# Kernel tuning notes

Hardware: AMD Instinct MI355X
Metric: run time of the kernel (lower is better)

## Reference

```python
import jax, jax.numpy as jnp
import numpy as np

NUM_GRAPHS = 1000


def _gine_conv(x, src, dst, edge_attr, w_e, b_e, w1, b1, w2, b2):
    # GINEConv (eps=0): out = nn(x + sum_{j->i} relu(x_j + lin_edge(e_ji)))
    e = edge_attr @ w_e + b_e                      # [E, F]
    m = jax.nn.relu(x[src] + e)                    # [E, F] per-edge message
    agg = jnp.zeros_like(x).at[dst].add(m)         # [N, F] scatter-add to targets
    h = x + agg
    h = jax.nn.relu(h @ w1 + b1)
    h = jax.nn.relu(h @ w2 + b2)
    return h


def _segment_softmax(scores, seg, num_segments):
    m = jax.ops.segment_max(scores, seg, num_segments=num_segments)
    z = jnp.exp(scores - m[seg])
    s = jax.ops.segment_sum(z, seg, num_segments=num_segments)
    return z / s[seg]


def setup_inputs() -> dict:
    key = jax.random.key(0)
    ks = jax.random.split(key, 16)
    N, E, F_IN, H, ED = 100000, 1600000, 9, 64, 1

    x = jax.random.normal(ks[0], (N, F_IN), dtype=jnp.float32)
    edge_index = jax.random.randint(ks[1], (2, E), 0, N, dtype=jnp.int32)
    edge_attr = jax.random.normal(ks[2], (E, ED), dtype=jnp.float32)
    batch = jnp.sort(jax.random.randint(ks[3], (N,), 0, NUM_GRAPHS, dtype=jnp.int32))
    B_total = jax.random.uniform(ks[4], (NUM_GRAPHS,), dtype=jnp.float32)

    def lin(k, fi, fo):
        k1, k2 = jax.random.split(k)
        bound = 1.0 / np.sqrt(fi)
        w = jax.random.uniform(k1, (fi, fo), minval=-bound, maxval=bound, dtype=jnp.float32)
        b = jax.random.uniform(k2, (fo,), minval=-bound, maxval=bound, dtype=jnp.float32)
        return w, b

    we1, be1 = lin(ks[5], ED, F_IN)    # conv1 edge projection -> in_channels
    w11, b11 = lin(ks[6], F_IN, H)
    w12, b12 = lin(ks[7], H, H)
    we2, be2 = lin(ks[8], ED, H)       # conv2 edge projection
    w21, b21 = lin(ks[9], H, H)
    w22, b22 = lin(ks[10], H, H)
    wr1, br1 = lin(ks[11], H, H // 2)
    wr2, br2 = lin(ks[12], H // 2, 1)

    return {"x": x, "edge_index": edge_index, "edge_attr": edge_attr,
            "batch": batch, "B_total": B_total,
            "we1": we1, "be1": be1, "w11": w11, "b11": b11, "w12": w12, "b12": b12,
            "we2": we2, "be2": be2, "w21": w21, "b21": b21, "w22": w22, "b22": b22,
            "wr1": wr1, "br1": br1, "wr2": wr2, "br2": br2}


def reference(x, edge_index, edge_attr, batch, B_total,
              we1, be1, w11, b11, w12, b12,
              we2, be2, w21, b21, w22, b22,
              wr1, br1, wr2, br2):
    src, dst = edge_index[0], edge_index[1]
    h = _gine_conv(x, src, dst, edge_attr, we1, be1, w11, b11, w12, b12)
    h = _gine_conv(h, src, dst, edge_attr, we2, be2, w21, b21, w22, b22)
    raw = (jax.nn.relu(h @ wr1 + br1) @ wr2 + br2)[:, 0]   # [N]
    alloc_probs = _segment_softmax(raw, batch, NUM_GRAPHS)
    return alloc_probs * B_total[batch]
```

## Files before the change

kernel.cpp:

```cpp
#include <hip/hip_runtime.h>
#include <float.h>

#define NBKCAP 128
#define EPB 8192

__device__ __forceinline__ unsigned short bf16rne(float f) {
  unsigned u = __float_as_uint(f);
  return (unsigned short)((u + 0x7FFFu + ((u >> 16) & 1u)) >> 16);
}

__global__ void bkhist_kernel(const int* __restrict__ dst, int* __restrict__ bkcount,
                              int E, int nbk) {
  __shared__ int lcnt[NBKCAP];
  for (int t = threadIdx.x; t < nbk; t += 256) lcnt[t] = 0;
  __syncthreads();
  for (int j = blockIdx.x * 256 + threadIdx.x; j < E; j += gridDim.x * 256)
    atomicAdd(&lcnt[dst[j] >> 10], 1);
  __syncthreads();
  for (int t = threadIdx.x; t < nbk; t += 256)
    if (lcnt[t]) atomicAdd(&bkcount[t], lcnt[t]);
}

__global__ void bkscan_kernel(const int* __restrict__ bkcount, int* __restrict__ bkbase,
                              int* __restrict__ bkcursor, int nbk, int E) {
  if (threadIdx.x == 0) {
    int run = 0;
    for (int i = 0; i < nbk; ++i) { bkbase[i] = run; bkcursor[i] = run; run += bkcount[i]; }
    bkbase[nbk] = E;
  }
}

__global__ void binA_kernel(const int* __restrict__ dst, const int* __restrict__ src,
                            const float* __restrict__ ea,
                            int* __restrict__ bkcursor, int4* __restrict__ epk4,
                            int E, int nbk) {
  __shared__ int lcnt[NBKCAP];
  __shared__ int lbase[NBKCAP];
  int e0 = blockIdx.x * EPB;
  int e1 = min(e0 + EPB, E);
  for (int t = threadIdx.x; t < nbk; t += 256) lcnt[t] = 0;
  __syncthreads();
  for (int j = e0 + threadIdx.x; j < e1; j += 256)
    atomicAdd(&lcnt[dst[j] >> 10], 1);
  __syncthreads();
  for (int t = threadIdx.x; t < nbk; t += 256) {
    int c = lcnt[t];
    lbase[t] = c ? atomicAdd(&bkcursor[t], c) : 0;
    lcnt[t] = 0;
  }
  __syncthreads();
  for (int j = e0 + threadIdx.x; j < e1; j += 256) {
    int d = dst[j];
    int bk = d >> 10;
    int ofs = atomicAdd(&lcnt[bk], 1);
    epk4[lbase[bk] + ofs] = make_int4(src[j], __float_as_int(ea[j]), d, 0);
  }
}

__global__ void bucket_build(const int4* __restrict__ epk4, const int* __restrict__ bkbase,
                             int* __restrict__ rowptr, int2* __restrict__ epack,
                             int N, int E) {
  __shared__ int ldeg[1024];
  __shared__ int lsum[256];
  int bk = blockIdx.x;
  int node0 = bk << 10;
  int s0 = bkbase[bk], s1 = bkbase[bk + 1];
  for (int t = threadIdx.x; t < 1024; t += 256) ldeg[t] = 0;
  __syncthreads();
  for (int p = s0 + threadIdx.x; p < s1; p += 256)
    atomicAdd(&ldeg[epk4[p].z & 1023], 1);
  __syncthreads();
  int base = threadIdx.x * 4;
  int v0 = ldeg[base], v1 = ldeg[base + 1], v2 = ldeg[base + 2], v3 = ldeg[base + 3];
  int s = v0 + v1 + v2 + v3;
  lsum[threadIdx.x] = s;
  __syncthreads();
  for (int off = 1; off < 256; off <<= 1) {
    int t = (threadIdx.x >= off) ? lsum[threadIdx.x - off] : 0;
    __syncthreads();
    lsum[threadIdx.x] += t;
    __syncthreads();
  }
  int ex = lsum[threadIdx.x] - s;
  __syncthreads();
  ldeg[base]     = s0 + ex;
  ldeg[base + 1] = s0 + ex + v0;
  ldeg[base + 2] = s0 + ex + v0 + v1;
  ldeg[base + 3] = s0 + ex + v0 + v1 + v2;
  __syncthreads();
  for (int t = threadIdx.x; t < 1024; t += 256) {
    int node = node0 + t;
    if (node < N) rowptr[node] = ldeg[t];
  }
  __syncthreads();
  for (int p = s0 + threadIdx.x; p < s1; p += 256) {
    int4 v = epk4[p];
    int pos = atomicAdd(&ldeg[v.z & 1023], 1);
    epack[pos] = make_int2(v.x, v.y);
  }
  if (bk == 0 && threadIdx.x == 0) rowptr[N] = E;
}

__global__ void __launch_bounds__(256, 8) gather1_kernel(
    const float* __restrict__ x, const int* __restrict__ rowptr,
    const int2* __restrict__ epack,
    const float* __restrict__ we1, const float* __restrict__ be1,
    float* __restrict__ xin, int N) {
  int i = blockIdx.x * blockDim.x + threadIdx.x;
  if (i >= N) return;
  float we[9], be[9];
#pragma unroll
  for (int f = 0; f < 9; ++f) { we[f] = we1[f]; be[f] = be1[f]; }
  float acc[9];
#pragma unroll
  for (int f = 0; f < 9; ++f) acc[f] = 0.0f;

  int p0 = rowptr[i], p1 = rowptr[i + 1];
  int p = p0;
  for (; p + 1 < p1; p += 2) {
    int2 e0 = epack[p], e1 = epack[p + 1];
    float a0 = __int_as_float(e0.y), a1 = __int_as_float(e1.y);
    float r0[9], r1[9];
#pragma unroll
    for (int f = 0; f < 9; ++f) r0[f] = x[(size_t)e0.x * 9 + f];
#pragma unroll
    for (int f = 0; f < 9; ++f) r1[f] = x[(size_t)e1.x * 9 + f];
#pragma unroll
    for (int f = 0; f < 9; ++f) {
      acc[f] += fmaxf(fmaf(a0, we[f], be[f]) + r0[f], 0.0f);
      acc[f] += fmaxf(fmaf(a1, we[f], be[f]) + r1[f], 0.0f);
    }
  }
  for (; p < p1; ++p) {
    int2 e = epack[p];
    float a = __int_as_float(e.y);
#pragma unroll
    for (int f = 0; f < 9; ++f)
      acc[f] += fmaxf(fmaf(a, we[f], be[f]) + x[(size_t)e.x * 9 + f], 0.0f);
  }
#pragma unroll
  for (int f = 0; f < 9; ++f) xin[(size_t)i * 9 + f] = x[(size_t)i * 9 + f] + acc[f];
}

__global__ void __launch_bounds__(256, 3) node1_mlp(
    const float* __restrict__ xin,
    const float* __restrict__ w11, const float* __restrict__ b11,
    const float* __restrict__ w12, const float* __restrict__ b12,
    unsigned short* __restrict__ h1b, int N) {
  __shared__ float sW1[9 * 64];
  __shared__ float sB1[64];
  __shared__ float sW2t[64 * 64];
  __shared__ float sB2[64];
  __shared__ unsigned short tile[256][66];
  for (int t = threadIdx.x; t < 9 * 64; t += blockDim.x) sW1[t] = w11[t];
  for (int t = threadIdx.x; t < 64 * 64; t += blockDim.x) {
    int o = t >> 6, k = t & 63;
    sW2t[t] = w12[k * 64 + o];
  }
  for (int t = threadIdx.x; t < 64; t += blockDim.x) { sB1[t] = b11[t]; sB2[t] = b12[t]; }
  __syncthreads();
  int i0 = blockIdx.x * 256;
  int i = i0 + threadIdx.x;
  if (i < N) {
    float xv[9];
#pragma unroll
    for (int k = 0; k < 9; ++k) xv[k] = xin[(size_t)i * 9 + k];
    float t1[64];
#pragma unroll
    for (int o = 0; o < 64; ++o) {
      float a = sB1[o];
#pragma unroll
      for (int k = 0; k < 9; ++k) a = fmaf(xv[k], sW1[k * 64 + o], a);
      t1[o] = fmaxf(a, 0.0f);
    }
#pragma unroll
    for (int o = 0; o < 64; ++o) {
      float a = sB2[o];
#pragma unroll
      for (int k = 0; k < 64; k += 4) {
        float4 wv = *(const float4*)(sW2t + o * 64 + k);
        a = fmaf(t1[k], wv.x, a);
        a = fmaf(t1[k + 1], wv.y, a);
        a = fmaf(t1[k + 2], wv.z, a);
        a = fmaf(t1[k + 3], wv.w, a);
      }
      tile[threadIdx.x][o] = bf16rne(fmaxf(a, 0.0f));
    }
  }
  __syncthreads();
#pragma unroll
  for (int it = 0; it < 16; ++it) {
    int idx = it * 256 + threadIdx.x;
    int r = idx >> 4;
    int c = idx & 15;
    if (i0 + r < N) {
      const unsigned short* tp = &tile[r][c * 4];
      uint2 v;
      v.x = (unsigned)tp[0] | ((unsigned)tp[1] << 16);
      v.y = (unsigned)tp[2] | ((unsigned)tp[3] << 16);
      *(uint2*)(h1b + (size_t)(i0 + r) * 64 + c * 4) = v;
    }
  }
}

__device__ __forceinline__ float4 bf4_to_f4(uint2 u) {
  float4 r;
  r.x = __uint_as_float(u.x << 16);
  r.y = __uint_as_float(u.x & 0xFFFF0000u);
  r.z = __uint_as_float(u.y << 16);
  r.w = __uint_as_float(u.y & 0xFFFF0000u);
  return r;
}

__global__ void __launch_bounds__(256, 8) gather2_kernel(
    const unsigned short* __restrict__ h1b, const int* __restrict__ rowptr,
    const int2* __restrict__ epack,
    const float* __restrict__ we2, const float* __restrict__ be2,
    float* __restrict__ agg2, int N) {
  int wid = threadIdx.x >> 6;
  int lane = threadIdx.x & 63;
  int g = lane >> 4;
  int l = lane & 15;
  int i = blockIdx.x * 4 + wid;
  if (i >= N) return;

  float4 we_l = *(const float4*)(we2 + 4 * l);
  float4 be_l = *(const float4*)(be2 + 4 * l);
  float4 acc = make_float4(0.f, 0.f, 0.f, 0.f);

  int p0 = rowptr[i], p1 = rowptr[i + 1];
  int p = p0 + g;
  for (; p + 4 < p1; p += 8) {
    int2 e0 = epack[p], e1 = epack[p + 4];
    float a0 = __int_as_float(e0.y), a1 = __int_as_float(e1.y);
    float4 h0 = bf4_to_f4(*(const uint2*)(h1b + (size_t)e0.x * 64 + 4 * l));
    float4 hv = bf4_to_f4(*(const uint2*)(h1b + (size_t)e1.x * 64 + 4 * l));
    acc.x += fmaxf(fmaf(a0, we_l.x, be_l.x) + h0.x, 0.f);
    acc.y += fmaxf(fmaf(a0, we_l.y, be_l.y) + h0.y, 0.f);
    acc.z += fmaxf(fmaf(a0, we_l.z, be_l.z) + h0.z, 0.f);
    acc.w += fmaxf(fmaf(a0, we_l.w, be_l.w) + h0.w, 0.f);
    acc.x += fmaxf(fmaf(a1, we_l.x, be_l.x) + hv.x, 0.f);
    acc.y += fmaxf(fmaf(a1, we_l.y, be_l.y) + hv.y, 0.f);
    acc.z += fmaxf(fmaf(a1, we_l.z, be_l.z) + hv.z, 0.f);
    acc.w += fmaxf(fmaf(a1, we_l.w, be_l.w) + hv.w, 0.f);
  }
  for (; p < p1; p += 4) {
    int2 e = epack[p];
    float a = __int_as_float(e.y);
    float4 h = bf4_to_f4(*(const uint2*)(h1b + (size_t)e.x * 64 + 4 * l));
    acc.x += fmaxf(fmaf(a, we_l.x, be_l.x) + h.x, 0.f);
    acc.y += fmaxf(fmaf(a, we_l.y, be_l.y) + h.y, 0.f);
    acc.z += fmaxf(fmaf(a, we_l.z, be_l.z) + h.z, 0.f);
    acc.w += fmaxf(fmaf(a, we_l.w, be_l.w) + h.w, 0.f);
  }
#pragma unroll
  for (int off = 16; off <= 32; off <<= 1) {
    acc.x += __shfl_xor(acc.x, off);
    acc.y += __shfl_xor(acc.y, off);
    acc.z += __shfl_xor(acc.z, off);
    acc.w += __shfl_xor(acc.w, off);
  }
  if (g == 0) {
    float4 hs = bf4_to_f4(*(const uint2*)(h1b + (size_t)i * 64 + 4 * l));
    acc.x += hs.x; acc.y += hs.y; acc.z += hs.z; acc.w += hs.w;
    *(float4*)(agg2 + (size_t)i * 64 + 4 * l) = acc;
  }
}

__global__ void __launch_bounds__(256, 2) node2_kernel(
    const float* __restrict__ agg2,
    const float* __restrict__ w21, const float* __restrict__ b21,
    const float* __restrict__ w22, const float* __restrict__ b22,
    const float* __restrict__ wr1, const float* __restrict__ br1,
    const float* __restrict__ wr2, const float* __restrict__ br2,
    float* __restrict__ raw, int N, int chunk) {
  __shared__ float sW1t[64 * 64];
  __shared__ float sW2t[64 * 64];
  __shared__ float sWr1t[32 * 64];
  __shared__ float sB1[64];
  __shared__ float sB2[64];
  __shared__ float sBr1[32];
  __shared__ float sWr2[32];
  __shared__ float sBr2;
  for (int t = threadIdx.x; t < 64 * 64; t += blockDim.x) {
    int o = t >> 6, k = t & 63;
    sW1t[t] = w21[k * 64 + o];
    sW2t[t] = w22[k * 64 + o];
  }
  for (int t = threadIdx.x; t < 32 * 64; t += blockDim.x) {
    int o = t >> 6, k = t & 63;
    sWr1t[t] = wr1[k * 32 + o];
  }
  for (int t = threadIdx.x; t < 64; t += blockDim.x) { sB1[t] = b21[t]; sB2[t] = b22[t]; }
  for (int t = threadIdx.x; t < 32; t += blockDim.x) { sBr1[t] = br1[t]; sWr2[t] = wr2[t]; }
  if (threadIdx.x == 0) sBr2 = br2[0];
  __syncthreads();
  int i = blockIdx.x * chunk + threadIdx.x;
  if ((int)threadIdx.x >= chunk || i >= N) return;
  float hin[64];
#pragma unroll
  for (int k = 0; k < 64; k += 4) {
    float4 v = *(const float4*)(agg2 + (size_t)i * 64 + k);
    hin[k] = v.x; hin[k + 1] = v.y; hin[k + 2] = v.z; hin[k + 3] = v.w;
  }
  float a1[64];
#pragma unroll
  for (int o = 0; o < 64; ++o) {
    float acc = sB1[o];
#pragma unroll
    for (int k = 0; k < 64; k += 4) {
      float4 wv = *(const float4*)(sW1t + o * 64 + k);
      acc = fmaf(hin[k], wv.x, acc);
      acc = fmaf(hin[k + 1], wv.y, acc);
      acc = fmaf(hin[k + 2], wv.z, acc);
      acc = fmaf(hin[k + 3], wv.w, acc);
    }
    a1[o] = fmaxf(acc, 0.0f);
  }
  float a2[64];
#pragma unroll
  for (int o = 0; o < 64; ++o) {
    float acc = sB2[o];
#pragma unroll
    for (int k = 0; k < 64; k += 4) {
      float4 wv = *(const float4*)(sW2t + o * 64 + k);
      acc = fmaf(a1[k], wv.x, acc);
      acc = fmaf(a1[k + 1], wv.y, acc);
      acc = fmaf(a1[k + 2], wv.z, acc);
      acc = fmaf(a1[k + 3], wv.w, acc);
    }
    a2[o] = fmaxf(acc, 0.0f);
  }
  float r[32];
#pragma unroll
  for (int o = 0; o < 32; ++o) {
    float acc = sBr1[o];
#pragma unroll
    for (int k = 0; k < 64; k += 4) {
      float4 wv = *(const float4*)(sWr1t + o * 64 + k);
      acc = fmaf(a2[k], wv.x, acc);
      acc = fmaf(a2[k + 1], wv.y, acc);
      acc = fmaf(a2[k + 2], wv.z, acc);
      acc = fmaf(a2[k + 3], wv.w, acc);
    }
    r[o] = fmaxf(acc, 0.0f);
  }
  float acc = sBr2;
#pragma unroll
  for (int k = 0; k < 32; ++k) acc = fmaf(r[k], sWr2[k], acc);
  raw[i] = acc;
}

__device__ __forceinline__ int lowerb(const int* __restrict__ a, int n, int key) {
  int lo = 0, hi = n;
  while (lo < hi) { int mid = (lo + hi) >> 1; if (a[mid] < key) lo = mid + 1; else hi = mid; }
  return lo;
}

__global__ void segsoftmax_kernel(const float* __restrict__ raw, const int* __restrict__ batch,
                                  const float* __restrict__ Btot, float* __restrict__ out, int N) {
  __shared__ float sred[256];
  int g = blockIdx.x;
  int tid = threadIdx.x;
  int start = lowerb(batch, N, g);
  int end = lowerb(batch, N, g + 1);
  if (start >= end) return;

  float m = -FLT_MAX;
  for (int i = start + tid; i < end; i += 256) m = fmaxf(m, raw[i]);
  sred[tid] = m;
  __syncthreads();
  for (int s = 128; s > 0; s >>= 1) {
    if (tid < s) sred[tid] = fmaxf(sred[tid], sred[tid + s]);
    __syncthreads();
  }
  m = sred[0];
  __syncthreads();

  float sum = 0.0f;
  for (int i = start + tid; i < end; i += 256) sum += expf(raw[i] - m);
  sred[tid] = sum;
  __syncthreads();
  for (int s = 128; s > 0; s >>= 1) {
    if (tid < s) sred[tid] += sred[tid + s];
    __syncthreads();
  }
  float scale = Btot[g] / sred[0];

  for (int i = start + tid; i < end; i += 256) out[i] = expf(raw[i] - m) * scale;
}

extern "C" void kernel_launch(void* const* d_in, const int* in_sizes, int n_in,
                              void* d_out, int out_size, void* d_ws, size_t ws_size,
                              hipStream_t stream) {
  const float* x     = (const float*)d_in[0];
  const int* eidx    = (const int*)d_in[1];
  const float* eattr = (const float*)d_in[2];
  const int* batch   = (const int*)d_in[3];
  const float* Btot  = (const float*)d_in[4];
  const float* we1 = (const float*)d_in[5];
  const float* be1 = (const float*)d_in[6];
  const float* w11 = (const float*)d_in[7];
  const float* b11 = (const float*)d_in[8];
  const float* w12 = (const float*)d_in[9];
  const float* b12 = (const float*)d_in[10];
  const float* we2 = (const float*)d_in[11];
  const float* be2 = (const float*)d_in[12];
  const float* w21 = (const float*)d_in[13];
  const float* b21 = (const float*)d_in[14];
  const float* w22 = (const float*)d_in[15];
  const float* b22 = (const float*)d_in[16];
  const float* wr1 = (const float*)d_in[17];
  const float* br1 = (const float*)d_in[18];
  const float* wr2 = (const float*)d_in[19];
  const float* br2 = (const float*)d_in[20];

  const int N  = in_sizes[0] / 9;
  const int E  = in_sizes[2];
  const int NG = in_sizes[4];
  const int* src = eidx;
  const int* dst = eidx + E;

  const int nbk = (N + 1023) >> 10;

  char* w = (char*)d_ws;
  int*   bkcount = (int*)w;                w += (size_t)NBKCAP * 4;
  int*   bkbase  = (int*)w;                w += (size_t)(NBKCAP + 1) * 4;
  int*   bkcursor = (int*)w;               w += (size_t)NBKCAP * 4;
  int*   rowptr = (int*)w;                 w += (size_t)(N + 1) * 4;
  int4*  epk4   = (int4*)w;                w += (size_t)E * 16;
  int2*  epack  = (int2*)w;                w += (size_t)E * 8;
  unsigned short* h1b = (unsigned short*)w; w += (size_t)N * 64 * 2;
  float* agg2   = (float*)w;               w += (size_t)N * 64 * 4;
  float* raw    = (float*)w;               w += (size_t)N * 4;
  float* xin = agg2;

  hipMemsetAsync(bkcount, 0, (size_t)NBKCAP * 4, stream);

  dim3 blk(256);
  dim3 ngrid((N + 255) / 256);

  bkhist_kernel<<<dim3(1024), blk, 0, stream>>>(dst, bkcount, E, nbk);
  bkscan_kernel<<<dim3(1), dim3(64), 0, stream>>>(bkcount, bkbase, bkcursor, nbk, E);
  binA_kernel<<<dim3((E + EPB - 1) / EPB), blk, 0, stream>>>(dst, src, eattr,
                                                             bkcursor, epk4, E, nbk);
  bucket_build<<<dim3(nbk), blk, 0, stream>>>(epk4, bkbase, rowptr, epack, N, E);

  gather1_kernel<<<ngrid, blk, 0, stream>>>(x, rowptr, epack, we1, be1, xin, N);
  node1_mlp<<<ngrid, blk, 0, stream>>>(xin, w11, b11, w12, b12, h1b, N);

  dim3 l2grid((N + 3) / 4);
  gather2_kernel<<<l2grid, blk, 0, stream>>>(h1b, rowptr, epack, we2, be2, agg2, N);
  const int N2B = 512;
  const int chunk = (N + N2B - 1) / N2B;
  node2_kernel<<<dim3(N2B), blk, 0, stream>>>(agg2, w21, b21, w22, b22,
                                              wr1, br1, wr2, br2, raw, N, chunk);

  segsoftmax_kernel<<<dim3(NG), blk, 0, stream>>>(raw, batch, Btot, (float*)d_out, N);
}
```

Before: 308.1 us.

## Fuse layer-2 edge gather with node MLP and readout via shared-memory tile

Merges the second-layer neighbor gather and the per-node MLP plus readout into one kernel. Each 256-thread block gathers 64 nodes into a shared tile, then 64 threads run the dense MLP from that tile, so the N×64 fp32 agg2 buffer is never written to or read back from global memory. The cost is that only one wavefront per block does the MLP while the other three sit idle. Occupancy also drops (launch bounds 2, large shared memory per block), which may hurt latency hiding in the gather phase. It launches 1563 blocks, where the old node kernel used 512.

```diff
diff --git a/kernel.cpp b/kernel.cpp
--- a/kernel.cpp
+++ b/kernel.cpp
@@ -212,68 +212,15 @@
   return r;
 }
 
-__global__ void __launch_bounds__(256, 8) gather2_kernel(
+__global__ void __launch_bounds__(256, 2) layer2_fused(
     const unsigned short* __restrict__ h1b, const int* __restrict__ rowptr,
     const int2* __restrict__ epack,
     const float* __restrict__ we2, const float* __restrict__ be2,
-    float* __restrict__ agg2, int N) {
-  int wid = threadIdx.x >> 6;
-  int lane = threadIdx.x & 63;
-  int g = lane >> 4;
-  int l = lane & 15;
-  int i = blockIdx.x * 4 + wid;
-  if (i >= N) return;
-
-  float4 we_l = *(const float4*)(we2 + 4 * l);
-  float4 be_l = *(const float4*)(be2 + 4 * l);
-  float4 acc = make_float4(0.f, 0.f, 0.f, 0.f);
-
-  int p0 = rowptr[i], p1 = rowptr[i + 1];
-  int p = p0 + g;
-  for (; p + 4 < p1; p += 8) {
-    int2 e0 = epack[p], e1 = epack[p + 4];
-    float a0 = __int_as_float(e0.y), a1 = __int_as_float(e1.y);
-    float4 h0 = bf4_to_f4(*(const uint2*)(h1b + (size_t)e0.x * 64 + 4 * l));
-    float4 hv = bf4_to_f4(*(const uint2*)(h1b + (size_t)e1.x * 64 + 4 * l));
-    acc.x += fmaxf(fmaf(a0, we_l.x, be_l.x) + h0.x, 0.f);
-    acc.y += fmaxf(fmaf(a0, we_l.y, be_l.y) + h0.y, 0.f);
-    acc.z += fmaxf(fmaf(a0, we_l.z, be_l.z) + h0.z, 0.f);
-    acc.w += fmaxf(fmaf(a0, we_l.w, be_l.w) + h0.w, 0.f);
-    acc.x += fmaxf(fmaf(a1, we_l.x, be_l.x) + hv.x, 0.f);
-    acc.y += fmaxf(fmaf(a1, we_l.y, be_l.y) + hv.y, 0.f);
-    acc.z += fmaxf(fmaf(a1, we_l.z, be_l.z) + hv.z, 0.f);
-    acc.w += fmaxf(fmaf(a1, we_l.w, be_l.w) + hv.w, 0.f);
-  }
-  for (; p < p1; p += 4) {
-    int2 e = epack[p];
-    float a = __int_as_float(e.y);
-    float4 h = bf4_to_f4(*(const uint2*)(h1b + (size_t)e.x * 64 + 4 * l));
-    acc.x += fmaxf(fmaf(a, we_l.x, be_l.x) + h.x, 0.f);
-    acc.y += fmaxf(fmaf(a, we_l.y, be_l.y) + h.y, 0.f);
-    acc.z += fmaxf(fmaf(a, we_l.z, be_l.z) + h.z, 0.f);
-    acc.w += fmaxf(fmaf(a, we_l.w, be_l.w) + h.w, 0.f);
-  }
-#pragma unroll
-  for (int off = 16; off <= 32; off <<= 1) {
-    acc.x += __shfl_xor(acc.x, off);
-    acc.y += __shfl_xor(acc.y, off);
-    acc.z += __shfl_xor(acc.z, off);
-    acc.w += __shfl_xor(acc.w, off);
-  }
-  if (g == 0) {
-    float4 hs = bf4_to_f4(*(const uint2*)(h1b + (size_t)i * 64 + 4 * l));
-    acc.x += hs.x; acc.y += hs.y; acc.z += hs.z; acc.w += hs.w;
-    *(float4*)(agg2 + (size_t)i * 64 + 4 * l) = acc;
-  }
-}
-
-__global__ void __launch_bounds__(256, 2) node2_kernel(
-    const float* __restrict__ agg2,
     const float* __restrict__ w21, const float* __restrict__ b21,
     const float* __restrict__ w22, const float* __restrict__ b22,
     const float* __restrict__ wr1, const float* __restrict__ br1,
     const float* __restrict__ wr2, const float* __restrict__ br2,
-    float* __restrict__ raw, int N, int chunk) {
+    float* __restrict__ raw, int N) {
   __shared__ float sW1t[64 * 64];
   __shared__ float sW2t[64 * 64];
   __shared__ float sWr1t[32 * 64];
@@ -282,73 +229,130 @@
   __shared__ float sBr1[32];
   __shared__ float sWr2[32];
   __shared__ float sBr2;
-  for (int t = threadIdx.x; t < 64 * 64; t += blockDim.x) {
+  __shared__ float tile[64][65];
+
+  for (int t = threadIdx.x; t < 64 * 64; t += 256) {
     int o = t >> 6, k = t & 63;
     sW1t[t] = w21[k * 64 + o];
     sW2t[t] = w22[k * 64 + o];
   }
-  for (int t = threadIdx.x; t < 32 * 64; t += blockDim.x) {
+  for (int t = threadIdx.x; t < 32 * 64; t += 256) {
     int o = t >> 6, k = t & 63;
     sWr1t[t] = wr1[k * 32 + o];
   }
-  for (int t = threadIdx.x; t < 64; t += blockDim.x) { sB1[t] = b21[t]; sB2[t] = b22[t]; }
-  for (int t = threadIdx.x; t < 32; t += blockDim.x) { sBr1[t] = br1[t]; sWr2[t] = wr2[t]; }
+  for (int t = threadIdx.x; t < 64; t += 256) { sB1[t] = b21[t]; sB2[t] = b22[t]; }
+  for (int t = threadIdx.x; t < 32; t += 256) { sBr1[t] = br1[t]; sWr2[t] = wr2[t]; }
   if (threadIdx.x == 0) sBr2 = br2[0];
-  __syncthreads();
-  int i = blockIdx.x * chunk + threadIdx.x;
-  if ((int)threadIdx.x >= chunk || i >= N) return;
-  float hin[64];
-#pragma unroll
-  for (int k = 0; k < 64; k += 4) {
-    float4 v = *(const float4*)(agg2 + (size_t)i * 64 + k);
-    hin[k] = v.x; hin[k + 1] = v.y; hin[k + 2] = v.z; hin[k + 3] = v.w;
-  }
-  float a1[64];
-#pragma unroll
-  for (int o = 0; o < 64; ++o) {
-    float acc = sB1[o];
-#pragma unroll
-    for (int k = 0; k < 64; k += 4) {
-      float4 wv = *(const float4*)(sW1t + o * 64 + k);
-      acc = fmaf(hin[k], wv.x, acc);
-      acc = fmaf(hin[k + 1], wv.y, acc);
-      acc = fmaf(hin[k + 2], wv.z, acc);
-      acc = fmaf(hin[k + 3], wv.w, acc);
-    }
-    a1[o] = fmaxf(acc, 0.0f);
-  }
-  float a2[64];
-#pragma unroll
-  for (int o = 0; o < 64; ++o) {
-    float acc = sB2[o];
-#pragma unroll
-    for (int k = 0; k < 64; k += 4) {
-      float4 wv = *(const float4*)(sW2t + o * 64 + k);
-      acc = fmaf(a1[k], wv.x, acc);
-      acc = fmaf(a1[k + 1], wv.y, acc);
-      acc = fmaf(a1[k + 2], wv.z, acc);
-      acc = fmaf(a1[k + 3], wv.w, acc);
-    }
-    a2[o] = fmaxf(acc, 0.0f);
-  }
-  float r[32];
-#pragma unroll
-  for (int o = 0; o < 32; ++o) {
-    float acc = sBr1[o];
-#pragma unroll
-    for (int k = 0; k < 64; k += 4) {
-      float4 wv = *(const float4*)(sWr1t + o * 64 + k);
-      acc = fmaf(a2[k], wv.x, acc);
-      acc = fmaf(a2[k + 1], wv.y, acc);
-      acc = fmaf(a2[k + 2], wv.z, acc);
-      acc = fmaf(a2[k + 3], wv.w, acc);
-    }
-    r[o] = fmaxf(acc, 0.0f);
-  }
-  float acc = sBr2;
-#pragma unroll
-  for (int k = 0; k < 32; ++k) acc = fmaf(r[k], sWr2[k], acc);
-  raw[i] = acc;
+
+  int wid = threadIdx.x >> 6;
+  int lane = threadIdx.x & 63;
+  int g = lane >> 4;
+  int l = lane & 15;
+  int base = blockIdx.x * 64;
+
+  float4 we_l = *(const float4*)(we2 + 4 * l);
+  float4 be_l = *(const float4*)(be2 + 4 * l);
+
+  for (int ni = 0; ni < 16; ++ni) {
+    int row = wid * 16 + ni;
+    int i = base + row;
+    if (i < N) {
+      float4 acc = make_float4(0.f, 0.f, 0.f, 0.f);
+      int p0 = rowptr[i], p1 = rowptr[i + 1];
+      int p = p0 + g;
+      for (; p + 4 < p1; p += 8) {
+        int2 e0 = epack[p], e1 = epack[p + 4];
+        float a0 = __int_as_float(e0.y), a1 = __int_as_float(e1.y);
+        float4 h0 = bf4_to_f4(*(const uint2*)(h1b + (size_t)e0.x * 64 + 4 * l));
+        float4 hv = bf4_to_f4(*(const uint2*)(h1b + (size_t)e1.x * 64 + 4 * l));
+        acc.x += fmaxf(fmaf(a0, we_l.x, be_l.x) + h0.x, 0.f);
+        acc.y += fmaxf(fmaf(a0, we_l.y, be_l.y) + h0.y, 0.f);
+        acc.z += fmaxf(fmaf(a0, we_l.z, be_l.z) + h0.z, 0.f);
+        acc.w += fmaxf(fmaf(a0, we_l.w, be_l.w) + h0.w, 0.f);
+        acc.x += fmaxf(fmaf(a1, we_l.x, be_l.x) + hv.x, 0.f);
+        acc.y += fmaxf(fmaf(a1, we_l.y, be_l.y) + hv.y, 0.f);
+        acc.z += fmaxf(fmaf(a1, we_l.z, be_l.z) + hv.z, 0.f);
+        acc.w += fmaxf(fmaf(a1, we_l.w, be_l.w) + hv.w, 0.f);
+      }
+      for (; p < p1; p += 4) {
+        int2 e = epack[p];
+        float a = __int_as_float(e.y);
+        float4 h = bf4_to_f4(*(const uint2*)(h1b + (size_t)e.x * 64 + 4 * l));
+        acc.x += fmaxf(fmaf(a, we_l.x, be_l.x) + h.x, 0.f);
+        acc.y += fmaxf(fmaf(a, we_l.y, be_l.y) + h.y, 0.f);
+        acc.z += fmaxf(fmaf(a, we_l.z, be_l.z) + h.z, 0.f);
+        acc.w += fmaxf(fmaf(a, we_l.w, be_l.w) + h.w, 0.f);
+      }
+#pragma unroll
+      for (int off = 16; off <= 32; off <<= 1) {
+        acc.x += __shfl_xor(acc.x, off);
+        acc.y += __shfl_xor(acc.y, off);
+        acc.z += __shfl_xor(acc.z, off);
+        acc.w += __shfl_xor(acc.w, off);
+      }
+      if (g == 0) {
+        float4 hs = bf4_to_f4(*(const uint2*)(h1b + (size_t)i * 64 + 4 * l));
+        tile[row][4 * l + 0] = acc.x + hs.x;
+        tile[row][4 * l + 1] = acc.y + hs.y;
+        tile[row][4 * l + 2] = acc.z + hs.z;
+        tile[row][4 * l + 3] = acc.w + hs.w;
+      }
+    }
+  }
+  __syncthreads();
+
+  int i = base + threadIdx.x;
+  if (threadIdx.x < 64 && i < N) {
+    float hin[64];
+#pragma unroll
+    for (int k = 0; k < 64; ++k) hin[k] = tile[threadIdx.x][k];
+    float a1[64];
+#pragma unroll
+    for (int o = 0; o < 64; ++o) {
+      float acc = sB1[o];
+#pragma unroll
+      for (int k = 0; k < 64; k += 4) {
+        float4 wv = *(const float4*)(sW1t + o * 64 + k);
+        acc = fmaf(hin[k], wv.x, acc);
+        acc = fmaf(hin[k + 1], wv.y, acc);
+        acc = fmaf(hin[k + 2], wv.z, acc);
+        acc = fmaf(hin[k + 3], wv.w, acc);
+      }
+      a1[o] = fmaxf(acc, 0.0f);
+    }
+    float a2[64];
+#pragma unroll
+    for (int o = 0; o < 64; ++o) {
+      float acc = sB2[o];
+#pragma unroll
+      for (int k = 0; k < 64; k += 4) {
+        float4 wv = *(const float4*)(sW2t + o * 64 + k);
+        acc = fmaf(a1[k], wv.x, acc);
+        acc = fmaf(a1[k + 1], wv.y, acc);
+        acc = fmaf(a1[k + 2], wv.z, acc);
+        acc = fmaf(a1[k + 3], wv.w, acc);
+      }
+      a2[o] = fmaxf(acc, 0.0f);
+    }
+    float r[32];
+#pragma unroll
+    for (int o = 0; o < 32; ++o) {
+      float acc = sBr1[o];
+#pragma unroll
+      for (int k = 0; k < 64; k += 4) {
+        float4 wv = *(const float4*)(sWr1t + o * 64 + k);
+        acc = fmaf(a2[k], wv.x, acc);
+        acc = fmaf(a2[k + 1], wv.y, acc);
+        acc = fmaf(a2[k + 2], wv.z, acc);
+        acc = fmaf(a2[k + 3], wv.w, acc);
+      }
+      r[o] = fmaxf(acc, 0.0f);
+    }
+    float acc = sBr2;
+#pragma unroll
+    for (int k = 0; k < 32; ++k) acc = fmaf(r[k], sWr2[k], acc);
+    raw[i] = acc;
+  }
 }
 
 __device__ __forceinline__ int lowerb(const int* __restrict__ a, int n, int key) {
@@ -431,9 +435,8 @@
   int4*  epk4   = (int4*)w;                w += (size_t)E * 16;
   int2*  epack  = (int2*)w;                w += (size_t)E * 8;
   unsigned short* h1b = (unsigned short*)w; w += (size_t)N * 64 * 2;
-  float* agg2   = (float*)w;               w += (size_t)N * 64 * 4;
+  float* xin    = (float*)w;               w += (size_t)N * 9 * 4;
   float* raw    = (float*)w;               w += (size_t)N * 4;
-  float* xin = agg2;
 
   hipMemsetAsync(bkcount, 0, (size_t)NBKCAP * 4, stream);
 
@@ -449,12 +452,10 @@
   gather1_kernel<<<ngrid, blk, 0, stream>>>(x, rowptr, epack, we1, be1, xin, N);
   node1_mlp<<<ngrid, blk, 0, stream>>>(xin, w11, b11, w12, b12, h1b, N);
 
-  dim3 l2grid((N + 3) / 4);
-  gather2_kernel<<<l2grid, blk, 0, stream>>>(h1b, rowptr, epack, we2, be2, agg2, N);
-  const int N2B = 512;
-  const int chunk = (N + N2B - 1) / N2B;
-  node2_kernel<<<dim3(N2B), blk, 0, stream>>>(agg2, w21, b21, w22, b22,
-                                              wr1, br1, wr2, br2, raw, N, chunk);
+  dim3 fgrid((N + 63) / 64);
+  layer2_fused<<<fgrid, blk, 0, stream>>>(h1b, rowptr, epack, we2, be2,
+                                          w21, b21, w22, b22, wr1, br1, wr2, br2,
+                                          raw, N);
 
   segsoftmax_kernel<<<dim3(NG), blk, 0, stream>>>(raw, batch, Btot, (float*)d_out, N);
 }
```

Result: slower. 560.6 us (+81.9%).
